# Kernel tuning notes

Measured on AMD Instinct MI355X. Metric: run time of the kernel, lower is better.

## Reference

```python
import jax, jax.numpy as jnp
import numpy as np

V, D, H, L, FF, B, S = 32000, 1024, 16, 4, 4096, 2, 1024
DK = D // H
STD = 0.02


def setup_inputs() -> dict:
    key = jax.random.key(0)
    ks = jax.random.split(key, 9)
    emb = jax.random.normal(ks[0], (V, D), jnp.float32) * STD
    w_qkv = jax.random.normal(ks[1], (L, D, 3 * D), jnp.float32) * STD
    w_o = jax.random.normal(ks[2], (L, D, D), jnp.float32) * STD
    w_gate = jax.random.normal(ks[3], (L, D, FF), jnp.float32) * STD
    w_up = jax.random.normal(ks[4], (L, D, FF), jnp.float32) * STD
    w_down = jax.random.normal(ks[5], (L, FF, D), jnp.float32) * STD
    norm1_w = jnp.ones((L, D), jnp.float32)
    norm2_w = jnp.ones((L, D), jnp.float32)
    final_norm_w = jnp.ones((D,), jnp.float32)
    input_ids = jax.random.randint(ks[6], (B, S), 0, V, dtype=jnp.int32)
    return dict(input_ids=input_ids, emb=emb, w_qkv=w_qkv, w_o=w_o,
                norm1_w=norm1_w, norm2_w=norm2_w,
                w_gate=w_gate, w_up=w_up, w_down=w_down,
                final_norm_w=final_norm_w)


def _rms(x, w, eps=1e-8):
    return w * x / jnp.sqrt(jnp.mean(x * x, axis=-1, keepdims=True) + eps)


def _rope_factor(seq_len, dk):
    # original: x_rope = x*cos + x*sin with cos/sin of shape [S, dk/2]
    # (duplicated along the feature dim to make the broadcast well-defined)
    pos = jnp.arange(seq_len, dtype=jnp.float32)
    freqs = jnp.exp(jnp.arange(0, dk, 2, dtype=jnp.float32) * (-jnp.log(10000.0) / dk))
    ang = pos[:, None] * freqs[None, :]                     # [S, dk/2]
    c = jnp.cos(ang); s = jnp.sin(ang)
    return jnp.concatenate([c, c], -1) + jnp.concatenate([s, s], -1)  # [S, dk]


def reference(input_ids, emb, w_qkv, w_o, norm1_w, norm2_w, w_gate, w_up, w_down, final_norm_w):
    b, s = input_ids.shape
    d = emb.shape[1]
    x = emb[input_ids] * jnp.sqrt(jnp.float32(d))           # [B,S,D]
    rope = _rope_factor(s, DK)                              # [S,DK]
    causal = jnp.tril(jnp.ones((s, s), bool))
    scale = 1.0 / jnp.sqrt(jnp.float32(DK))

    def block(x, p):
        wqkv, wo, n1, n2, wg, wu, wd = p
        nx = _rms(x, n1)
        qkv = (nx @ wqkv).reshape(b, s, 3, H, DK).transpose(2, 0, 3, 1, 4)  # [3,B,H,S,DK]
        q, k, v = qkv[0], qkv[1], qkv[2]
        q = q * rope
        k = k * rope
        scores = jnp.einsum('bhsd,bhtd->bhst', q, k) * scale
        scores = jnp.where(causal, scores, jnp.float32(-1e9))
        attn = jax.nn.softmax(scores, axis=-1)
        o = jnp.einsum('bhst,bhtd->bhsd', attn, v)
        o = o.transpose(0, 2, 1, 3).reshape(b, s, d)
        x = x + o @ wo
        nx = _rms(x, n2)
        ff = (jax.nn.silu(nx @ wg) * (nx @ wu)) @ wd
        return x + ff, None

    x, _ = jax.lax.scan(block, x, (w_qkv, w_o, norm1_w, norm2_w, w_gate, w_up, w_down))
    x = _rms(x, final_norm_w)
    logits = x @ emb.T                                      # tied lm_head
    return logits
```

## Files before the change

kernel.cpp:

```cpp
#include <hip/hip_runtime.h>
#include <hip/hip_bf16.h>
#include <math.h>

#define B_ 2
#define S_ 1024
#define D_ 1024
#define H_ 16
#define DK_ 64
#define L_ 4
#define FF_ 4096
#define V_ 32000
#define NT (B_*S_)

typedef __attribute__((ext_vector_type(8))) short short8v;
typedef __attribute__((ext_vector_type(4))) float floatx4;
typedef __hip_bfloat16 bf16;

__device__ inline float b2f(unsigned short u) {
  unsigned v = ((unsigned)u) << 16;
  float f; __builtin_memcpy(&f, &v, 4); return f;
}
__device__ inline unsigned short f2bu(float f) {
  bf16 h = __float2bfloat16(f);
  unsigned short u; __builtin_memcpy(&u, &h, 2); return u;
}

__global__ __launch_bounds__(256) void k_embed(const int* __restrict__ ids,
    const float* __restrict__ emb, float* __restrict__ x) {
  int i = blockIdx.x*256 + threadIdx.x;
  if (i >= NT*D_) return;
  int tok = i >> 10;
  int d = i & 1023;
  x[i] = emb[(size_t)ids[tok]*D_ + d] * 32.0f;
}

__global__ __launch_bounds__(256) void k_rms(const float* __restrict__ x,
    const float* __restrict__ w, bf16* __restrict__ o) {
  int row = blockIdx.x;
  const float* xr = x + (size_t)row*D_;
  float s = 0.f;
  for (int d = threadIdx.x; d < D_; d += 256) { float v = xr[d]; s += v*v; }
  for (int off = 32; off; off >>= 1) s += __shfl_down(s, off);
  __shared__ float red[4];
  __shared__ float inv_s;
  int wid = threadIdx.x >> 6;
  if ((threadIdx.x & 63) == 0) red[wid] = s;
  __syncthreads();
  if (threadIdx.x == 0) {
    float t = red[0]+red[1]+red[2]+red[3];
    inv_s = 1.0f / sqrtf(t * (1.0f/D_) + 1e-8f);
  }
  __syncthreads();
  float inv = inv_s;
  bf16* orow = o + (size_t)row*D_;
  for (int d = threadIdx.x; d < D_; d += 256) orow[d] = __float2bfloat16(w[d]*xr[d]*inv);
}

__global__ __launch_bounds__(256) void k_transpose_cast(const float* __restrict__ src0,
    bf16* __restrict__ dst0, int K, int N, size_t src_stride, size_t dst_stride) {
  const float* src = src0 + blockIdx.z * src_stride;
  bf16* dst = dst0 + blockIdx.z * dst_stride;
  __shared__ float t[64][65];
  int k0 = blockIdx.y*64, n0 = blockIdx.x*64;
  int r  = threadIdx.x >> 4;
  int c4 = (threadIdx.x & 15)*4;
  #pragma unroll
  for (int i = 0; i < 4; ++i) {
    float4 v = *(const float4*)(src + (size_t)(k0 + r + i*16)*N + n0 + c4);
    t[r+i*16][c4] = v.x; t[r+i*16][c4+1] = v.y;
    t[r+i*16][c4+2] = v.z; t[r+i*16][c4+3] = v.w;
  }
  __syncthreads();
  int nn = threadIdx.x >> 2;
  int kc = threadIdx.x & 3;
  #pragma unroll
  for (int i = 0; i < 4; ++i) {
    int kk = kc*4 + i*16;
    ushort4 o;
    o.x = f2bu(t[kk][nn]);   o.y = f2bu(t[kk+1][nn]);
    o.z = f2bu(t[kk+2][nn]); o.w = f2bu(t[kk+3][nn]);
    *(ushort4*)(dst + (size_t)(n0+nn)*K + k0 + kk) = o;
  }
}

__global__ __launch_bounds__(256) void k_cast4(const float* __restrict__ s,
    bf16* __restrict__ d, int n4) {
  int i = blockIdx.x*256 + threadIdx.x;
  if (i >= n4) return;
  float4 v = ((const float4*)s)[i];
  ushort4 o;
  o.x = f2bu(v.x); o.y = f2bu(v.y); o.z = f2bu(v.z); o.w = f2bu(v.w);
  ((ushort4*)d)[i] = o;
}

template<int EPI, bool OUTBF>
__global__ __launch_bounds__(256) void k_mfma_gemm_bt(
    const bf16* __restrict__ A, const bf16* __restrict__ Bt,
    const void* __restrict__ aux, void* __restrict__ Cout,
    int M, int N, int K) {
  const int NM = M >> 7, NN = N >> 7;
  const int wg = blockIdx.x;
  const int grp = wg >> 3, xcd = wg & 7;
  const int mi = grp % NM;
  const int ni = xcd + 8*(grp / NM);
  if (ni >= NN) return;
  const int bm = mi * 128;
  const int bn = ni * 128;

  __shared__ bf16 As[128*32];
  __shared__ bf16 Bs[128*32];
  const int tid  = threadIdx.x;
  const int lane = tid & 63;
  const int wave = tid >> 6;
  const int wm = (wave >> 1) * 64;
  const int wn = (wave & 1) * 64;

  floatx4 acc[4][4] = {};

  for (int k0 = 0; k0 < K; k0 += 32) {
    #pragma unroll
    for (int c = 0; c < 2; ++c) {
      int e = (c*256 + tid) * 8;
      int row = e >> 5, col = e & 31;
      const bf16* ga = A  + (size_t)(bm + row)*K + k0 + col;
      const bf16* gb = Bt + (size_t)(bn + row)*K + k0 + col;
      int ldsoff = (c*256 + wave*64) * 8;
      __builtin_amdgcn_global_load_lds(
        (const __attribute__((address_space(1))) void*)ga,
        (__attribute__((address_space(3))) void*)(As + ldsoff), 16, 0, 0);
      __builtin_amdgcn_global_load_lds(
        (const __attribute__((address_space(1))) void*)gb,
        (__attribute__((address_space(3))) void*)(Bs + ldsoff), 16, 0, 0);
    }
    __syncthreads();
    const int r = lane & 15, kc = lane >> 4;
    short8v a[4], b[4];
    #pragma unroll
    for (int i = 0; i < 4; ++i) {
      a[i] = *(const short8v*)(As + (size_t)(wm + i*16 + r)*32 + kc*8);
      b[i] = *(const short8v*)(Bs + (size_t)(wn + i*16 + r)*32 + kc*8);
    }
    #pragma unroll
    for (int i = 0; i < 4; ++i)
      #pragma unroll
      for (int j = 0; j < 4; ++j)
        acc[i][j] = __builtin_amdgcn_mfma_f32_16x16x32_bf16(a[i], b[j], acc[i][j], 0, 0, 0);
    __syncthreads();
  }

  const int cn = lane & 15, rq = lane >> 4;
  #pragma unroll
  for (int i=0;i<4;i++) {
    #pragma unroll
    for (int j=0;j<4;j++) {
      const int gcol = bn + wn + j*16 + cn;
      float freq = 0.f;
      if constexpr (EPI==2) {
        if (gcol < 2048)
          freq = expf((float)(gcol & 31) * -0.28782313662425574f);
      }
      #pragma unroll
      for (int rr=0; rr<4; ++rr) {
        const int grow = bm + wm + i*16 + rq*4 + rr;
        const size_t off = (size_t)grow*N + gcol;
        float v = acc[i][j][rr];
        if constexpr (EPI==1) v += ((const float*)aux)[off];
        if constexpr (EPI==2) {
          if (gcol < 2048) {
            float sn, cs;
            sincosf((float)(grow & 1023) * freq, &sn, &cs);
            v *= (cs + sn);
          }
        }
        if constexpr (EPI==3) {
          float gv = b2f(((const unsigned short*)aux)[off]);
          v *= gv / (1.0f + expf(-gv));
        }
        if constexpr (OUTBF) ((bf16*)Cout)[off] = __float2bfloat16(v);
        else                 ((float*)Cout)[off] = v;
      }
    }
  }
}

static inline int remap_grid(int M, int N) {
  int NM = M >> 7, NN = N >> 7;
  int NN8 = (NN + 7) & ~7;
  return NM * NN8;
}

__global__ __launch_bounds__(256) void k_gemm_64(
    const bf16* __restrict__ A, const bf16* __restrict__ Bt,
    const float* __restrict__ res, float* __restrict__ C,
    int M, int N, int K) {
  const int NN = N >> 7;
  const int nwg = gridDim.x;
  const int id = (blockIdx.x & 7)*(nwg >> 3) + (blockIdx.x >> 3);
  const int mi = id / NN, ni = id % NN;
  const int bm = mi << 6, bn = ni << 7;

  __shared__ bf16 As[64*32];
  __shared__ bf16 Bs[128*32];
  const int tid  = threadIdx.x;
  const int lane = tid & 63;
  const int wave = tid >> 6;
  const int wm = (wave >> 1) * 32;
  const int wn = (wave & 1) * 64;

  floatx4 acc[2][4] = {};

  for (int k0 = 0; k0 < K; k0 += 32) {
    {
      int row = tid >> 2, col = (tid & 3)*8;
      const bf16* ga = A + (size_t)(bm + row)*K + k0 + col;
      __builtin_amdgcn_global_load_lds(
        (const __attribute__((address_space(1))) void*)ga,
        (__attribute__((address_space(3))) void*)(As + wave*512), 16, 0, 0);
    }
    #pragma unroll
    for (int c = 0; c < 2; ++c) {
      int i = c*256 + tid;
      int row = i >> 2, col = (i & 3)*8;
      const bf16* gb = Bt + (size_t)(bn + row)*K + k0 + col;
      __builtin_amdgcn_global_load_lds(
        (const __attribute__((address_space(1))) void*)gb,
        (__attribute__((address_space(3))) void*)(Bs + (c*256 + wave*64)*8), 16, 0, 0);
    }
    __syncthreads();
    const int r = lane & 15, kc = lane >> 4;
    short8v a[2], b[4];
    #pragma unroll
    for (int i = 0; i < 2; ++i)
      a[i] = *(const short8v*)(As + (size_t)(wm + i*16 + r)*32 + kc*8);
    #pragma unroll
    for (int j = 0; j < 4; ++j)
      b[j] = *(const short8v*)(Bs + (size_t)(wn + j*16 + r)*32 + kc*8);
    #pragma unroll
    for (int i = 0; i < 2; ++i)
      #pragma unroll
      for (int j = 0; j < 4; ++j)
        acc[i][j] = __builtin_amdgcn_mfma_f32_16x16x32_bf16(a[i], b[j], acc[i][j], 0, 0, 0);
    __syncthreads();
  }

  const int cn = lane & 15, rq = lane >> 4;
  #pragma unroll
  for (int i = 0; i < 2; ++i) {
    #pragma unroll
    for (int j = 0; j < 4; ++j) {
      #pragma unroll
      for (int rr = 0; rr < 4; ++rr) {
        int grow = bm + wm + i*16 + rq*4 + rr;
        int gcol = bn + wn + j*16 + cn;
        size_t off = (size_t)grow*N + gcol;
        C[off] = acc[i][j][rr] + res[off];
      }
    }
  }
}

__global__ __launch_bounds__(512, 2) void k_gemm256(
    const bf16* __restrict__ A, const bf16* __restrict__ Bt,
    float* __restrict__ C, int M, int N, int K) {
  const int NM = M >> 8;
  const int nwg = gridDim.x;
  const int id = (blockIdx.x & 7)*(nwg >> 3) + (blockIdx.x >> 3);
  const int mi = id % NM, ni = id / NM;
  const int bm = mi << 8, bn = ni << 8;

  __shared__ bf16 As3[3][256*32];
  __shared__ bf16 Bs3[3][256*32];

  const int tid  = threadIdx.x;
  const int lane = tid & 63;
  const int wave = tid >> 6;
  const int wr = wave >> 2;
  const int wc = wave & 3;
  const int fr = lane & 15;
  const int kc = lane >> 4;

  floatx4 acc[8][4] = {};

  const int ntk = K >> 5;

  auto stage = [&](int kt, int slot) {
    const bf16* Ab = A  + (size_t)bm*K + kt*32;
    const bf16* Bb = Bt + (size_t)bn*K + kt*32;
    #pragma unroll
    for (int c = 0; c < 2; ++c) {
      int i = c*512 + tid;
      int row = i >> 2, sl = i & 3;
      int gcol = (sl ^ ((row >> 1) & 3)) * 8;
      int ldsoff = (c*512 + wave*64) * 8;
      __builtin_amdgcn_global_load_lds(
        (const __attribute__((address_space(1))) void*)(Ab + (size_t)row*K + gcol),
        (__attribute__((address_space(3))) void*)(&As3[slot][ldsoff]), 16, 0, 0);
      __builtin_amdgcn_global_load_lds(
        (const __attribute__((address_space(1))) void*)(Bb + (size_t)row*K + gcol),
        (__attribute__((address_space(3))) void*)(&Bs3[slot][ldsoff]), 16, 0, 0);
    }
  };

  stage(0, 0);
  if (ntk > 1) stage(1, 1);

  for (int t = 0; t < ntk; ++t) {
    const int cur = t % 3;
    __builtin_amdgcn_sched_barrier(0);
    __builtin_amdgcn_s_barrier();
    __builtin_amdgcn_sched_barrier(0);
    if (t + 2 < ntk) {
      stage(t + 2, (t + 2) % 3);
      __builtin_amdgcn_sched_barrier(0);
      asm volatile("s_waitcnt vmcnt(8)" ::: "memory");
    } else if (t + 1 < ntk) {
      asm volatile("s_waitcnt vmcnt(4)" ::: "memory");
    } else {
      asm volatile("s_waitcnt vmcnt(0)" ::: "memory");
    }
    __builtin_amdgcn_sched_barrier(0);
    __builtin_amdgcn_s_barrier();
    __builtin_amdgcn_sched_barrier(0);

    const bf16* Ab = As3[cur];
    const bf16* Bb = Bs3[cur];
    short8v a[8], b[4];
    #pragma unroll
    for (int f = 0; f < 8; ++f) {
      int r = wr*128 + f*16 + fr;
      int sl = kc ^ ((r >> 1) & 3);
      a[f] = *(const short8v*)(Ab + r*32 + sl*8);
    }
    #pragma unroll
    for (int f = 0; f < 4; ++f) {
      int r = wc*64 + f*16 + fr;
      int sl = kc ^ ((r >> 1) & 3);
      b[f] = *(const short8v*)(Bb + r*32 + sl*8);
    }
    __builtin_amdgcn_s_setprio(1);
    #pragma unroll
    for (int f = 0; f < 8; ++f)
      #pragma unroll
      for (int j = 0; j < 4; ++j)
        acc[f][j] = __builtin_amdgcn_mfma_f32_16x16x32_bf16(a[f], b[j], acc[f][j], 0, 0, 0);
    __builtin_amdgcn_s_setprio(0);
  }

  const int cn = lane & 15, rq = lane >> 4;
  #pragma unroll
  for (int f = 0; f < 8; ++f) {
    #pragma unroll
    for (int j = 0; j < 4; ++j) {
      #pragma unroll
      for (int rr = 0; rr < 4; ++rr) {
        int row = bm + wr*128 + f*16 + rq*4 + rr;
        int col = bn + wc*64 + j*16 + cn;
        C[(size_t)row*N + col] = acc[f][j][rr];
      }
    }
  }
}

__global__ __launch_bounds__(256) void k_fattn(const bf16* __restrict__ qkvb,
    bf16* __restrict__ outb) {
  const unsigned short* qkv = (const unsigned short*)qkvb;
  const int qt = 15 - blockIdx.x;
  const int h = blockIdx.y, b = blockIdx.z;
  const int tid = threadIdx.x, lane = tid & 63, w = tid >> 6;
  const int g = lane >> 4, qn = lane & 15;

  __shared__ unsigned short Ks[64*64];
  __shared__ unsigned short Vt[64*64];
  __shared__ unsigned short Ps[4*16*64];

  const int q0 = qt * 64;
  const int qw0 = q0 + w*16;

  short8v qf[2];
  {
    const unsigned short* qp = qkv + ((size_t)(b*S_ + qw0 + qn))*3072 + h*DK_ + g*8;
    qf[0] = *(const short8v*)qp;
    qf[1] = *(const short8v*)(qp + 32);
  }

  floatx4 o_acc[4] = {};
  float m_run = -1e30f, l_run = 0.f;

  const int ntile = qt + 1;
  for (int it = 0; it < ntile; ++it) {
    const int t0 = it*64;

    {
      const int trow = w*8 + (lane>>3);
      const int d16 = (lane&7) ^ (trow&7);
      #pragma unroll
      for (int c = 0; c < 2; ++c) {
        const unsigned short* gk = qkv + ((size_t)(b*S_ + t0 + c*32 + trow))*3072
                                   + 1024 + h*DK_ + d16*8;
        __builtin_amdgcn_global_load_lds(
          (const __attribute__((address_space(1))) void*)gk,
          (__attribute__((address_space(3))) void*)(Ks + c*2048 + w*512), 16, 0, 0);
      }
    }
    #pragma unroll
    for (int c = 0; c < 2; ++c) {
      int idx = c*256 + tid;
      int t = idx >> 3;
      int d0 = (idx & 7)*8;
      short8v vv = *(const short8v*)(qkv + ((size_t)(b*S_ + t0 + t))*3072 + 2048 + h*DK_ + d0);
      #pragma unroll
      for (int jj = 0; jj < 8; ++jj) {
        int d = d0 + jj;
        int slot = ((t>>3) ^ (d&7) ^ ((d>>3)&7)) & 7;
        Vt[d*64 + slot*8 + (t&7)] = (unsigned short)vv[jj];
      }
    }
    __syncthreads();

    floatx4 st[4];
    #pragma unroll
    for (int f = 0; f < 4; ++f) {
      st[f] = (floatx4){0.f,0.f,0.f,0.f};
      int t = f*16 + qn;
      #pragma unroll
      for (int ks = 0; ks < 2; ++ks) {
        int slot = ((ks*4 + g) ^ (t&7)) & 7;
        short8v kf = *(const short8v*)(Ks + t*64 + slot*8);
        st[f] = __builtin_amdgcn_mfma_f32_16x16x32_bf16(kf, qf[ks], st[f], 0,0,0);
      }
    }

    const bool diag = (it == qt);
    float sc[4][4];
    #pragma unroll
    for (int f = 0; f < 4; ++f)
      #pragma unroll
      for (int r = 0; r < 4; ++r) {
        float v = st[f][r]*0.125f;
        if (diag) {
          int tl = f*16 + g*4 + r;
          if (tl > w*16 + qn) v = -1e30f;
        }
        sc[f][r] = v;
      }
    float mx = -1e30f;
    #pragma unroll
    for (int f = 0; f < 4; ++f)
      #pragma unroll
      for (int r = 0; r < 4; ++r) mx = fmaxf(mx, sc[f][r]);
    mx = fmaxf(mx, __shfl_xor(mx, 16));
    mx = fmaxf(mx, __shfl_xor(mx, 32));
    float m_new = fmaxf(m_run, mx);
    float corr = __expf(m_run - m_new);
    m_run = m_new;
    float ls = 0.f;
    #pragma unroll
    for (int f = 0; f < 4; ++f)
      #pragma unroll
      for (int r = 0; r < 4; ++r) {
        float p = __expf(sc[f][r] - m_new);
        sc[f][r] = p;
        ls += p;
      }
    ls += __shfl_xor(ls, 16);
    ls += __shfl_xor(ls, 32);
    l_run = l_run*corr + ls;

    unsigned short* Pw = Ps + w*1024;
    #pragma unroll
    for (int f = 0; f < 4; ++f) {
      unsigned int lo = (unsigned int)f2bu(sc[f][0]) | ((unsigned int)f2bu(sc[f][1]) << 16);
      unsigned int hi = (unsigned int)f2bu(sc[f][2]) | ((unsigned int)f2bu(sc[f][3]) << 16);
      int c16 = f*2 + (g>>1);
      int slot = (c16 ^ (qn&7)) & 7;
      *(uint2*)((char*)Pw + qn*128 + slot*16 + (g&1)*8) = make_uint2(lo, hi);
    }

    #pragma unroll
    for (int r = 0; r < 4; ++r) {
      float cr = __shfl(corr, g*4 + r);
      #pragma unroll
      for (int fd = 0; fd < 4; ++fd) o_acc[fd][r] *= cr;
    }

    short8v pf[2];
    #pragma unroll
    for (int ks = 0; ks < 2; ++ks) {
      int slot = ((ks*4 + g) ^ (qn&7)) & 7;
      pf[ks] = *(const short8v*)(Pw + qn*64 + slot*8);
    }
    #pragma unroll
    for (int fd = 0; fd < 4; ++fd) {
      int d = fd*16 + qn;
      #pragma unroll
      for (int ks = 0; ks < 2; ++ks) {
        int slot = ((ks*4 + g) ^ (d&7) ^ ((d>>3)&7)) & 7;
        short8v vf = *(const short8v*)(Vt + d*64 + slot*8);
        o_acc[fd] = __builtin_amdgcn_mfma_f32_16x16x32_bf16(pf[ks], vf, o_acc[fd], 0,0,0);
      }
    }
    __syncthreads();
  }

  float linv = 1.0f / l_run;
  #pragma unroll
  for (int r = 0; r < 4; ++r) {
    float li = __shfl(linv, g*4 + r);
    int row = qw0 + g*4 + r;
    bf16* op = outb + (size_t)(b*S_ + row)*D_ + h*DK_ + qn;
    #pragma unroll
    for (int fd = 0; fd < 4; ++fd)
      op[fd*16] = __float2bfloat16(o_acc[fd][r] * li);
  }
}

extern "C" void kernel_launch(void* const* d_in, const int* in_sizes, int n_in,
                              void* d_out, int out_size, void* d_ws, size_t ws_size,
                              hipStream_t stream) {
  (void)in_sizes; (void)n_in; (void)out_size; (void)ws_size;
  const int*   ids  = (const int*)d_in[0];
  const float* emb  = (const float*)d_in[1];
  const float* wqkv = (const float*)d_in[2];
  const float* wo   = (const float*)d_in[3];
  const float* n1   = (const float*)d_in[4];
  const float* n2   = (const float*)d_in[5];
  const float* wg   = (const float*)d_in[6];
  const float* wu   = (const float*)d_in[7];
  const float* wd   = (const float*)d_in[8];
  const float* fnw  = (const float*)d_in[9];
  float* out = (float*)d_out;

  char* ws = (char*)d_ws;
  float* x      = (float*)ws;                                   ws += (size_t)NT*D_*4;
  bf16*  nx_bf  = (bf16*)ws;                                    ws += (size_t)NT*D_*2;
  bf16*  att_bf = (bf16*)ws;                                    ws += (size_t)NT*D_*2;
  bf16*  shared = (bf16*)ws;                                    ws += (size_t)2*NT*FF_*2;
  bf16*  emb_bf = (bf16*)ws;                                    ws += (size_t)V_*D_*2;
  bf16*  qkv_bf = shared;
  bf16*  g_bf   = shared;

  bf16* wsc = (bf16*)d_out;
  bf16* wqkv_t = wsc;
  bf16* wo_t   = wqkv_t + (size_t)L_*3*D_*D_;
  bf16* wg_t   = wo_t   + (size_t)L_*D_*D_;
  bf16* wu_t   = wg_t   + (size_t)L_*D_*FF_;
  bf16* wd_t   = wu_t   + (size_t)L_*D_*FF_;

  dim3 blk(256);

  {
    dim3 gq(3*D_/64, D_/64, L_);
    k_transpose_cast<<<gq, blk, 0, stream>>>(wqkv, wqkv_t, D_, 3*D_,
        (size_t)D_*3*D_, (size_t)3*D_*D_);
    dim3 go(D_/64, D_/64, L_);
    k_transpose_cast<<<go, blk, 0, stream>>>(wo, wo_t, D_, D_,
        (size_t)D_*D_, (size_t)D_*D_);
    dim3 gg(FF_/64, D_/64, L_);
    k_transpose_cast<<<gg, blk, 0, stream>>>(wg, wg_t, D_, FF_,
        (size_t)D_*FF_, (size_t)D_*FF_);
    k_transpose_cast<<<gg, blk, 0, stream>>>(wu, wu_t, D_, FF_,
        (size_t)D_*FF_, (size_t)D_*FF_);
    dim3 gdn(D_/64, FF_/64, L_);
    k_transpose_cast<<<gdn, blk, 0, stream>>>(wd, wd_t, FF_, D_,
        (size_t)FF_*D_, (size_t)D_*FF_);
  }
  k_cast4<<<(V_*D_/4 + 255)/256, blk, 0, stream>>>(emb, emb_bf, V_*D_/4);

  k_embed<<<(NT*D_+255)/256, blk, 0, stream>>>(ids, emb, x);

  for (int l = 0; l < L_; ++l) {
    k_rms<<<NT, blk, 0, stream>>>(x, n1 + (size_t)l*D_, nx_bf);
    k_mfma_gemm_bt<2,true><<<remap_grid(NT,3*D_), blk, 0, stream>>>(
        nx_bf, wqkv_t + (size_t)l*3*D_*D_, nullptr, qkv_bf, NT, 3*D_, D_);
    dim3 gattn(16, H_, B_);
    k_fattn<<<gattn, blk, 0, stream>>>(qkv_bf, att_bf);
    k_gemm_64<<<(NT/64)*(D_/128), blk, 0, stream>>>(
        att_bf, wo_t + (size_t)l*D_*D_, x, x, NT, D_, D_);
    k_rms<<<NT, blk, 0, stream>>>(x, n2 + (size_t)l*D_, nx_bf);
    k_mfma_gemm_bt<0,true><<<remap_grid(NT,FF_), blk, 0, stream>>>(
        nx_bf, wg_t + (size_t)l*D_*FF_, nullptr, g_bf, NT, FF_, D_);
    k_mfma_gemm_bt<3,true><<<remap_grid(NT,FF_), blk, 0, stream>>>(
        nx_bf, wu_t + (size_t)l*D_*FF_, g_bf, g_bf, NT, FF_, D_);
    k_gemm_64<<<(NT/64)*(D_/128), blk, 0, stream>>>(
        g_bf, wd_t + (size_t)l*D_*FF_, x, x, NT, D_, FF_);
  }
  k_rms<<<NT, blk, 0, stream>>>(x, fnw, nx_bf);
  k_gemm256<<<(NT/256)*(V_/256), dim3(512), 0, stream>>>(
      nx_bf, emb_bf, out, NT, V_, D_);
}
```

Measured before the change: 1.409 ms.

## Fuse gate/up GEMMs into one wide GEMM and double-buffer gemm256

Gate and up weights are concatenated into a single [2*FF, D] matrix, so one 256x256-tile GEMM produces both projections into an NT x 8192 buffer. A separate elementwise kernel then applies silu(gate)*up in place, and the down projection reads it through a new lda stride. k_gemm256 is also changed from a triple-buffered pipeline with fine-grained vmcnt waits to a simple double buffer with a full wait each step, and its launch bounds are raised to 4 blocks per CU. This removes one GEMM launch and the re-read of nx, but adds an extra pass over the gate/up buffer and may weaken load/compute overlap in the logits GEMM.

```diff
diff --git a/kernel.cpp b/kernel.cpp
--- a/kernel.cpp
+++ b/kernel.cpp
@@ -172,10 +172,6 @@
             v *= (cs + sn);
           }
         }
-        if constexpr (EPI==3) {
-          float gv = b2f(((const unsigned short*)aux)[off]);
-          v *= gv / (1.0f + expf(-gv));
-        }
         if constexpr (OUTBF) ((bf16*)Cout)[off] = __float2bfloat16(v);
         else                 ((float*)Cout)[off] = v;
       }
@@ -192,7 +188,7 @@
 __global__ __launch_bounds__(256) void k_gemm_64(
     const bf16* __restrict__ A, const bf16* __restrict__ Bt,
     const float* __restrict__ res, float* __restrict__ C,
-    int M, int N, int K) {
+    int M, int N, int K, int lda) {
   const int NN = N >> 7;
   const int nwg = gridDim.x;
   const int id = (blockIdx.x & 7)*(nwg >> 3) + (blockIdx.x >> 3);
@@ -212,7 +208,7 @@
   for (int k0 = 0; k0 < K; k0 += 32) {
     {
       int row = tid >> 2, col = (tid & 3)*8;
-      const bf16* ga = A + (size_t)(bm + row)*K + k0 + col;
+      const bf16* ga = A + (size_t)(bm + row)*lda + k0 + col;
       __builtin_amdgcn_global_load_lds(
         (const __attribute__((address_space(1))) void*)ga,
         (__attribute__((address_space(3))) void*)(As + wave*512), 16, 0, 0);
@@ -259,17 +255,18 @@
   }
 }
 
-__global__ __launch_bounds__(512, 2) void k_gemm256(
+template<bool OUTBF>
+__global__ __launch_bounds__(512, 4) void k_gemm256(
     const bf16* __restrict__ A, const bf16* __restrict__ Bt,
-    float* __restrict__ C, int M, int N, int K) {
+    void* __restrict__ C, int M, int N, int K) {
   const int NM = M >> 8;
   const int nwg = gridDim.x;
   const int id = (blockIdx.x & 7)*(nwg >> 3) + (blockIdx.x >> 3);
   const int mi = id % NM, ni = id / NM;
   const int bm = mi << 8, bn = ni << 8;
 
-  __shared__ bf16 As3[3][256*32];
-  __shared__ bf16 Bs3[3][256*32];
+  __shared__ bf16 As2[2][256*32];
+  __shared__ bf16 Bs2[2][256*32];
 
   const int tid  = threadIdx.x;
   const int lane = tid & 63;
@@ -280,7 +277,6 @@
   const int kc = lane >> 4;
 
   floatx4 acc[8][4] = {};
-
   const int ntk = K >> 5;
 
   auto stage = [&](int kt, int slot) {
@@ -294,36 +290,23 @@
       int ldsoff = (c*512 + wave*64) * 8;
       __builtin_amdgcn_global_load_lds(
         (const __attribute__((address_space(1))) void*)(Ab + (size_t)row*K + gcol),
-        (__attribute__((address_space(3))) void*)(&As3[slot][ldsoff]), 16, 0, 0);
+        (__attribute__((address_space(3))) void*)(&As2[slot][ldsoff]), 16, 0, 0);
       __builtin_amdgcn_global_load_lds(
         (const __attribute__((address_space(1))) void*)(Bb + (size_t)row*K + gcol),
-        (__attribute__((address_space(3))) void*)(&Bs3[slot][ldsoff]), 16, 0, 0);
+        (__attribute__((address_space(3))) void*)(&Bs2[slot][ldsoff]), 16, 0, 0);
     }
   };
 
   stage(0, 0);
-  if (ntk > 1) stage(1, 1);
-
+  asm volatile("s_waitcnt vmcnt(0)" ::: "memory");
+  __builtin_amdgcn_s_barrier();
+
+  int cur = 0;
   for (int t = 0; t < ntk; ++t) {
-    const int cur = t % 3;
-    __builtin_amdgcn_sched_barrier(0);
-    __builtin_amdgcn_s_barrier();
-    __builtin_amdgcn_sched_barrier(0);
-    if (t + 2 < ntk) {
-      stage(t + 2, (t + 2) % 3);
-      __builtin_amdgcn_sched_barrier(0);
-      asm volatile("s_waitcnt vmcnt(8)" ::: "memory");
-    } else if (t + 1 < ntk) {
-      asm volatile("s_waitcnt vmcnt(4)" ::: "memory");
-    } else {
-      asm volatile("s_waitcnt vmcnt(0)" ::: "memory");
-    }
-    __builtin_amdgcn_sched_barrier(0);
-    __builtin_amdgcn_s_barrier();
-    __builtin_amdgcn_sched_barrier(0);
-
-    const bf16* Ab = As3[cur];
-    const bf16* Bb = Bs3[cur];
+    if (t + 1 < ntk) stage(t + 1, cur ^ 1);
+
+    const bf16* Ab = As2[cur];
+    const bf16* Bb = Bs2[cur];
     short8v a[8], b[4];
     #pragma unroll
     for (int f = 0; f < 8; ++f) {
@@ -344,6 +327,10 @@
       for (int j = 0; j < 4; ++j)
         acc[f][j] = __builtin_amdgcn_mfma_f32_16x16x32_bf16(a[f], b[j], acc[f][j], 0, 0, 0);
     __builtin_amdgcn_s_setprio(0);
+
+    asm volatile("s_waitcnt vmcnt(0)" ::: "memory");
+    __builtin_amdgcn_s_barrier();
+    cur ^= 1;
   }
 
   const int cn = lane & 15, rq = lane >> 4;
@@ -355,10 +342,30 @@
       for (int rr = 0; rr < 4; ++rr) {
         int row = bm + wr*128 + f*16 + rq*4 + rr;
         int col = bn + wc*64 + j*16 + cn;
-        C[(size_t)row*N + col] = acc[f][j][rr];
-      }
-    }
-  }
+        size_t off = (size_t)row*N + col;
+        if constexpr (OUTBF) ((bf16*)C)[off] = __float2bfloat16(acc[f][j][rr]);
+        else                 ((float*)C)[off] = acc[f][j][rr];
+      }
+    }
+  }
+}
+
+__global__ __launch_bounds__(256) void k_silumul_gu(bf16* __restrict__ gu) {
+  int i = blockIdx.x*256 + threadIdx.x;
+  if (i >= NT*512) return;
+  int row = i >> 9;
+  int c8 = (i & 511)*8;
+  unsigned short* p = (unsigned short*)gu + (size_t)row*8192 + c8;
+  short8v g = *(const short8v*)p;
+  short8v u = *(const short8v*)(p + 4096);
+  short8v o;
+  #pragma unroll
+  for (int j = 0; j < 8; ++j) {
+    float gf = b2f((unsigned short)g[j]);
+    float uf = b2f((unsigned short)u[j]);
+    o[j] = (short)f2bu(gf / (1.0f + expf(-gf)) * uf);
+  }
+  *(short8v*)p = o;
 }
 
 __global__ __launch_bounds__(256) void k_fattn(const bf16* __restrict__ qkvb,
@@ -534,17 +541,16 @@
   float* x      = (float*)ws;                                   ws += (size_t)NT*D_*4;
   bf16*  nx_bf  = (bf16*)ws;                                    ws += (size_t)NT*D_*2;
   bf16*  att_bf = (bf16*)ws;                                    ws += (size_t)NT*D_*2;
-  bf16*  shared = (bf16*)ws;                                    ws += (size_t)2*NT*FF_*2;
+  bf16*  shared = (bf16*)ws;                                    ws += (size_t)NT*8192*2;
   bf16*  emb_bf = (bf16*)ws;                                    ws += (size_t)V_*D_*2;
   bf16*  qkv_bf = shared;
-  bf16*  g_bf   = shared;
+  bf16*  gu     = shared;
 
   bf16* wsc = (bf16*)d_out;
   bf16* wqkv_t = wsc;
   bf16* wo_t   = wqkv_t + (size_t)L_*3*D_*D_;
-  bf16* wg_t   = wo_t   + (size_t)L_*D_*D_;
-  bf16* wu_t   = wg_t   + (size_t)L_*D_*FF_;
-  bf16* wd_t   = wu_t   + (size_t)L_*D_*FF_;
+  bf16* wgu_t  = wo_t   + (size_t)L_*D_*D_;
+  bf16* wd_t   = wgu_t  + (size_t)L_*2*D_*FF_;
 
   dim3 blk(256);
 
@@ -556,10 +562,10 @@
     k_transpose_cast<<<go, blk, 0, stream>>>(wo, wo_t, D_, D_,
         (size_t)D_*D_, (size_t)D_*D_);
     dim3 gg(FF_/64, D_/64, L_);
-    k_transpose_cast<<<gg, blk, 0, stream>>>(wg, wg_t, D_, FF_,
-        (size_t)D_*FF_, (size_t)D_*FF_);
-    k_transpose_cast<<<gg, blk, 0, stream>>>(wu, wu_t, D_, FF_,
-        (size_t)D_*FF_, (size_t)D_*FF_);
+    k_transpose_cast<<<gg, blk, 0, stream>>>(wg, wgu_t, D_, FF_,
+        (size_t)D_*FF_, (size_t)2*D_*FF_);
+    k_transpose_cast<<<gg, blk, 0, stream>>>(wu, wgu_t + (size_t)FF_*D_, D_, FF_,
+        (size_t)D_*FF_, (size_t)2*D_*FF_);
     dim3 gdn(D_/64, FF_/64, L_);
     k_transpose_cast<<<gdn, blk, 0, stream>>>(wd, wd_t, FF_, D_,
         (size_t)FF_*D_, (size_t)D_*FF_);
@@ -575,16 +581,15 @@
     dim3 gattn(16, H_, B_);
     k_fattn<<<gattn, blk, 0, stream>>>(qkv_bf, att_bf);
     k_gemm_64<<<(NT/64)*(D_/128), blk, 0, stream>>>(
-        att_bf, wo_t + (size_t)l*D_*D_, x, x, NT, D_, D_);
+        att_bf, wo_t + (size_t)l*D_*D_, x, x, NT, D_, D_, D_);
     k_rms<<<NT, blk, 0, stream>>>(x, n2 + (size_t)l*D_, nx_bf);
-    k_mfma_gemm_bt<0,true><<<remap_grid(NT,FF_), blk, 0, stream>>>(
-        nx_bf, wg_t + (size_t)l*D_*FF_, nullptr, g_bf, NT, FF_, D_);
-    k_mfma_gemm_bt<3,true><<<remap_grid(NT,FF_), blk, 0, stream>>>(
-        nx_bf, wu_t + (size_t)l*D_*FF_, g_bf, g_bf, NT, FF_, D_);
+    k_gemm256<true><<<(NT/256)*(2*FF_/256), dim3(512), 0, stream>>>(
+        nx_bf, wgu_t + (size_t)l*2*D_*FF_, gu, NT, 2*FF_, D_);
+    k_silumul_gu<<<(NT*512 + 255)/256, blk, 0, stream>>>(gu);
     k_gemm_64<<<(NT/64)*(D_/128), blk, 0, stream>>>(
-        g_bf, wd_t + (size_t)l*D_*FF_, x, x, NT, D_, FF_);
+        gu, wd_t + (size_t)l*D_*FF_, x, x, NT, D_, FF_, 2*FF_);
   }
   k_rms<<<NT, blk, 0, stream>>>(x, fnw, nx_bf);
-  k_gemm256<<<(NT/256)*(V_/256), dim3(512), 0, stream>>>(
+  k_gemm256<false><<<(NT/256)*(V_/256), dim3(512), 0, stream>>>(
       nx_bf, emb_bf, out, NT, V_, D_);
 }
```

Result: slower. 3.812 ms (+170.6%).
